# Performance work log

Hardware: AMD Instinct MI355X
Metric: run time of the kernel (lower is better)

Reference implementation:

```python
import jax, jax.numpy as jnp
import numpy as np

IN_FEATURES = 5
OUT_FEATURES = 10
BITS = 2
N_TOKENS = 4_000_000


def fake_quant_weight(w, bits):
    # Symmetric per-output-channel quantization.
    # levels: qmin = -2^(b-1), qmax = 2^(b-1)-1  (for bits=2: {-2,-1,0,1})
    qmax = 2 ** (bits - 1) - 1
    qmin = -(2 ** (bits - 1))
    # per-row (per output channel) scale; avoid div-by-zero
    scale = jnp.max(jnp.abs(w), axis=1, keepdims=True) / qmax  # [out, 1]
    scale = jnp.maximum(scale, 1e-8)
    w_q = jnp.clip(jnp.round(w / scale), qmin, qmax)
    return w_q * scale  # dequantized weight, [out, in]


def setup_inputs() -> dict:
    key = jax.random.key(0)
    kx, kw, kb = jax.random.split(key, 3)
    x = jax.random.normal(kx, (N_TOKENS, IN_FEATURES), dtype=jnp.float32)
    # Kaiming-uniform-ish init like nn.Linear
    bound = 1.0 / np.sqrt(IN_FEATURES)
    weight = jax.random.uniform(kw, (OUT_FEATURES, IN_FEATURES), dtype=jnp.float32,
                                minval=-bound, maxval=bound)
    bias = jax.random.uniform(kb, (OUT_FEATURES,), dtype=jnp.float32,
                              minval=-bound, maxval=bound)
    return {"x": x, "weight": weight, "bias": bias}


def reference(x, weight, bias):
    # QuantizedLinear(5, 10, bits=2): 2-bit fake-quantized weight matmul + bias.
    w_deq = fake_quant_weight(weight, BITS)            # [out, in]
    return x @ w_deq.T + bias                          # [N, out]
```

## Files before the change

### kernel.cpp

```cpp
#include <hip/hip_runtime.h>


constexpr int IN_F = 5;
constexpr int OUT_F = 10;
constexpr int BLOCK = 256;
constexpr int TOK_PER_TILE = 1024;

__global__ __launch_bounds__(BLOCK) void qlinear_kernel(
    const float* __restrict__ x,
    const float* __restrict__ w,
    const float* __restrict__ bias,
    float* __restrict__ out,
    int n_tokens)
{
    __shared__ float wdq[OUT_F * IN_F];
    __shared__ float bsh[OUT_F];
    __shared__ float xs[TOK_PER_TILE * IN_F];
    __shared__ float os[TOK_PER_TILE * OUT_F];

    const int tid = threadIdx.x;

    if (tid < OUT_F) {
        float row[IN_F];
        float mx = 0.0f;
        #pragma unroll
        for (int j = 0; j < IN_F; ++j) {
            row[j] = w[tid * IN_F + j];
            mx = fmaxf(mx, fabsf(row[j]));
        }
        float scale = fmaxf(mx, 1e-8f);
        #pragma unroll
        for (int j = 0; j < IN_F; ++j) {
            float q = rintf(row[j] / scale);
            q = fminf(fmaxf(q, -2.0f), 1.0f);
            wdq[tid * IN_F + j] = q * scale;
        }
        bsh[tid] = bias[tid];
    }
    __syncthreads();

    const long tok0 = (long)blockIdx.x * TOK_PER_TILE;
    const bool full = (tok0 + TOK_PER_TILE) <= (long)n_tokens;

    const long xbase = tok0 * IN_F;
    if (full) {
        const float4* __restrict__ xg = (const float4*)(x + xbase);
        float4* xls = (float4*)xs;
        #pragma unroll
        for (int k = 0; k < (TOK_PER_TILE * IN_F / 4) / BLOCK; ++k)
            xls[tid + k * BLOCK] = xg[tid + k * BLOCK];
    } else {
        const long xtotal = (long)n_tokens * IN_F;
        for (int k = tid; k < TOK_PER_TILE * IN_F; k += BLOCK) {
            long gi = xbase + k;
            xs[k] = (gi < xtotal) ? x[gi] : 0.0f;
        }
    }
    __syncthreads();

    #pragma unroll
    for (int m = 0; m < TOK_PER_TILE / BLOCK; ++m) {
        const int lt = tid + m * BLOCK;
        float xv[IN_F];
        #pragma unroll
        for (int j = 0; j < IN_F; ++j) xv[j] = xs[lt * IN_F + j];
        #pragma unroll
        for (int o = 0; o < OUT_F; ++o) {
            float acc = bsh[o];
            #pragma unroll
            for (int j = 0; j < IN_F; ++j)
                acc = fmaf(xv[j], wdq[o * IN_F + j], acc);
            os[lt * OUT_F + o] = acc;
        }
    }
    __syncthreads();

    const long obase = tok0 * OUT_F;
    if (full) {
        const float4* ols = (const float4*)os;
        float4* __restrict__ og = (float4*)(out + obase);
        #pragma unroll
        for (int k = 0; k < (TOK_PER_TILE * OUT_F / 4) / BLOCK; ++k)
            og[tid + k * BLOCK] = ols[tid + k * BLOCK];
    } else {
        const long ototal = (long)n_tokens * OUT_F;
        for (int k = tid; k < TOK_PER_TILE * OUT_F; k += BLOCK) {
            long gi = obase + k;
            if (gi < ototal) out[gi] = os[k];
        }
    }
}

extern "C" void kernel_launch(void* const* d_in, const int* in_sizes, int n_in,
                              void* d_out, int out_size, void* d_ws, size_t ws_size,
                              hipStream_t stream) {
    const float* x    = (const float*)d_in[0];
    const float* wgt  = (const float*)d_in[1];
    const float* bias = (const float*)d_in[2];
    float* out = (float*)d_out;

    const int n_tokens = in_sizes[0] / IN_F;
    const int tiles = (n_tokens + TOK_PER_TILE - 1) / TOK_PER_TILE;

    qlinear_kernel<<<tiles, BLOCK, 0, stream>>>(x, wgt, bias, out, n_tokens);
}
```

Measured before the change: 225.0 us.

## Replace shared-memory tiling with per-thread two-token register computation

Removes the shared-memory staging of input and output tiles and has each thread load two tokens' inputs directly with float2 loads, compute both outputs in registers, and write them with float4 stores. This aims to cut the large LDS footprint that limited occupancy and to eliminate block barriers. Global accesses become strided per thread rather than fully coalesced, and an odd trailing token would no longer be processed.

```diff
diff --git a/kernel.cpp b/kernel.cpp
--- a/kernel.cpp
+++ b/kernel.cpp
@@ -1,94 +1,73 @@
 #include <hip/hip_runtime.h>
 
 
-constexpr int IN_F = 5;
+constexpr int IN_F  = 5;
 constexpr int OUT_F = 10;
 constexpr int BLOCK = 256;
-constexpr int TOK_PER_TILE = 1024;
 
 __global__ __launch_bounds__(BLOCK) void qlinear_kernel(
     const float* __restrict__ x,
     const float* __restrict__ w,
     const float* __restrict__ bias,
     float* __restrict__ out,
-    int n_tokens)
+    int n_pairs)
 {
     __shared__ float wdq[OUT_F * IN_F];
     __shared__ float bsh[OUT_F];
-    __shared__ float xs[TOK_PER_TILE * IN_F];
-    __shared__ float os[TOK_PER_TILE * OUT_F];
 
-    const int tid = threadIdx.x;
-
-    if (tid < OUT_F) {
+    if (threadIdx.x < OUT_F) {
+        const int o = threadIdx.x;
         float row[IN_F];
         float mx = 0.0f;
         #pragma unroll
         for (int j = 0; j < IN_F; ++j) {
-            row[j] = w[tid * IN_F + j];
+            row[j] = w[o * IN_F + j];
             mx = fmaxf(mx, fabsf(row[j]));
         }
-        float scale = fmaxf(mx, 1e-8f);
+        const float scale = fmaxf(mx, 1e-8f);
         #pragma unroll
         for (int j = 0; j < IN_F; ++j) {
             float q = rintf(row[j] / scale);
             q = fminf(fmaxf(q, -2.0f), 1.0f);
-            wdq[tid * IN_F + j] = q * scale;
+            wdq[o * IN_F + j] = q * scale;
         }
-        bsh[tid] = bias[tid];
+        bsh[o] = bias[o];
     }
     __syncthreads();
 
-    const long tok0 = (long)blockIdx.x * TOK_PER_TILE;
-    const bool full = (tok0 + TOK_PER_TILE) <= (long)n_tokens;
+    const int p = blockIdx.x * BLOCK + threadIdx.x;
+    if (p >= n_pairs) return;
 
-    const long xbase = tok0 * IN_F;
-    if (full) {
-        const float4* __restrict__ xg = (const float4*)(x + xbase);
-        float4* xls = (float4*)xs;
+    const float2* __restrict__ xg = (const float2*)(x + (long)p * (2 * IN_F));
+    float xv[2 * IN_F];
+    #pragma unroll
+    for (int k = 0; k < IN_F; ++k) {
+        float2 v = xg[k];
+        xv[2 * k]     = v.x;
+        xv[2 * k + 1] = v.y;
+    }
+
+    float o0[OUT_F], o1[OUT_F];
+    #pragma unroll
+    for (int o = 0; o < OUT_F; ++o) {
+        float a0 = bsh[o];
+        float a1 = a0;
         #pragma unroll
-        for (int k = 0; k < (TOK_PER_TILE * IN_F / 4) / BLOCK; ++k)
-            xls[tid + k * BLOCK] = xg[tid + k * BLOCK];
-    } else {
-        const long xtotal = (long)n_tokens * IN_F;
-        for (int k = tid; k < TOK_PER_TILE * IN_F; k += BLOCK) {
-            long gi = xbase + k;
-            xs[k] = (gi < xtotal) ? x[gi] : 0.0f;
+        for (int j = 0; j < IN_F; ++j) {
+            const float wv = wdq[o * IN_F + j];
+            a0 = fmaf(xv[j],         wv, a0);
+            a1 = fmaf(xv[IN_F + j],  wv, a1);
         }
+        o0[o] = a0;
+        o1[o] = a1;
     }
-    __syncthreads();
 
-    #pragma unroll
-    for (int m = 0; m < TOK_PER_TILE / BLOCK; ++m) {
-        const int lt = tid + m * BLOCK;
-        float xv[IN_F];
-        #pragma unroll
-        for (int j = 0; j < IN_F; ++j) xv[j] = xs[lt * IN_F + j];
-        #pragma unroll
-        for (int o = 0; o < OUT_F; ++o) {
-            float acc = bsh[o];
-            #pragma unroll
-            for (int j = 0; j < IN_F; ++j)
-                acc = fmaf(xv[j], wdq[o * IN_F + j], acc);
-            os[lt * OUT_F + o] = acc;
-        }
-    }
-    __syncthreads();
-
-    const long obase = tok0 * OUT_F;
-    if (full) {
-        const float4* ols = (const float4*)os;
-        float4* __restrict__ og = (float4*)(out + obase);
-        #pragma unroll
-        for (int k = 0; k < (TOK_PER_TILE * OUT_F / 4) / BLOCK; ++k)
-            og[tid + k * BLOCK] = ols[tid + k * BLOCK];
-    } else {
-        const long ototal = (long)n_tokens * OUT_F;
-        for (int k = tid; k < TOK_PER_TILE * OUT_F; k += BLOCK) {
-            long gi = obase + k;
-            if (gi < ototal) out[gi] = os[k];
-        }
-    }
+    float4* __restrict__ og = (float4*)(out + (long)p * (2 * OUT_F));
+    og[0] = make_float4(o0[0], o0[1], o0[2], o0[3]);
+    og[1] = make_float4(o0[4], o0[5], o0[6], o0[7]);
+    og[2] = make_float4(o0[8], o0[9], o1[0], o1[1]);
+    og[3] = make_float4(o1[2], o1[3], o1[4], o1[5]);
+    og[4] = make_float4(o1[6], o1[7], o1[8], o1[9]);
 }
 
 extern "C" void kernel_launch(void* const* d_in, const int* in_sizes, int n_in,
@@ -100,7 +79,8 @@
     float* out = (float*)d_out;
 
     const int n_tokens = in_sizes[0] / IN_F;
-    const int tiles = (n_tokens + TOK_PER_TILE - 1) / TOK_PER_TILE;
+    const int n_pairs  = n_tokens / 2;
+    const int blocks   = (n_pairs + BLOCK - 1) / BLOCK;
 
-    qlinear_kernel<<<tiles, BLOCK, 0, stream>>>(x, wgt, bias, out, n_tokens);
+    qlinear_kernel<<<blocks, BLOCK, 0, stream>>>(x, wgt, bias, out, n_pairs);
 }
```

Measured after the change: 236.7 us. +5.2%, slower.

## Shrink tiles to one token per thread and use nontemporal scalar accesses

Applied to the files above, without the earlier changes.

Cuts the per-block tile from 1024 to 256 tokens, so each thread handles a single token. This reduces shared memory per block from about 60KB to about 15KB, which should let many more blocks stay resident per CU and hide memory latency better. Global loads and stores become scalar nontemporal accesses instead of float4 copies, to keep streaming data out of the cache. The separate barrier after the weight dequantization is folded into the barrier after the x load. The tradeoffs are narrower memory instructions, more blocks to launch and the weight preprocessing being repeated in four times as many blocks.

```diff
diff --git a/kernel.cpp b/kernel.cpp
--- a/kernel.cpp
+++ b/kernel.cpp
@@ -1,10 +1,10 @@
 #include <hip/hip_runtime.h>
 
 
-constexpr int IN_F = 5;
+constexpr int IN_F  = 5;
 constexpr int OUT_F = 10;
 constexpr int BLOCK = 256;
-constexpr int TOK_PER_TILE = 1024;
+constexpr int TOK   = 256;
 
 __global__ __launch_bounds__(BLOCK) void qlinear_kernel(
     const float* __restrict__ x,
@@ -15,8 +15,8 @@
 {
     __shared__ float wdq[OUT_F * IN_F];
     __shared__ float bsh[OUT_F];
-    __shared__ float xs[TOK_PER_TILE * IN_F];
-    __shared__ float os[TOK_PER_TILE * OUT_F];
+    __shared__ float xs[TOK * IN_F];
+    __shared__ float os[TOK * OUT_F];
 
     const int tid = threadIdx.x;
 
@@ -28,7 +28,7 @@
             row[j] = w[tid * IN_F + j];
             mx = fmaxf(mx, fabsf(row[j]));
         }
-        float scale = fmaxf(mx, 1e-8f);
+        const float scale = fmaxf(mx, 1e-8f);
         #pragma unroll
         for (int j = 0; j < IN_F; ++j) {
             float q = rintf(row[j] / scale);
@@ -37,55 +37,56 @@
         }
         bsh[tid] = bias[tid];
     }
-    __syncthreads();
 
-    const long tok0 = (long)blockIdx.x * TOK_PER_TILE;
-    const bool full = (tok0 + TOK_PER_TILE) <= (long)n_tokens;
+    const long tok0 = (long)blockIdx.x * TOK;
+    const bool full = (tok0 + TOK) <= (long)n_tokens;
+    const long xbase = tok0 * IN_F;
+    const long obase = tok0 * OUT_F;
 
-    const long xbase = tok0 * IN_F;
     if (full) {
-        const float4* __restrict__ xg = (const float4*)(x + xbase);
-        float4* xls = (float4*)xs;
         #pragma unroll
-        for (int k = 0; k < (TOK_PER_TILE * IN_F / 4) / BLOCK; ++k)
-            xls[tid + k * BLOCK] = xg[tid + k * BLOCK];
+        for (int i = 0; i < IN_F; ++i) {
+            const int k = i * BLOCK + tid;
+            xs[k] = __builtin_nontemporal_load(x + xbase + k);
+        }
     } else {
         const long xtotal = (long)n_tokens * IN_F;
-        for (int k = tid; k < TOK_PER_TILE * IN_F; k += BLOCK) {
-            long gi = xbase + k;
+        #pragma unroll
+        for (int i = 0; i < IN_F; ++i) {
+            const int k = i * BLOCK + tid;
+            const long gi = xbase + k;
             xs[k] = (gi < xtotal) ? x[gi] : 0.0f;
         }
     }
     __syncthreads();
 
-    #pragma unroll
-    for (int m = 0; m < TOK_PER_TILE / BLOCK; ++m) {
-        const int lt = tid + m * BLOCK;
+    {
         float xv[IN_F];
         #pragma unroll
-        for (int j = 0; j < IN_F; ++j) xv[j] = xs[lt * IN_F + j];
+        for (int j = 0; j < IN_F; ++j) xv[j] = xs[tid * IN_F + j];
         #pragma unroll
         for (int o = 0; o < OUT_F; ++o) {
             float acc = bsh[o];
             #pragma unroll
             for (int j = 0; j < IN_F; ++j)
                 acc = fmaf(xv[j], wdq[o * IN_F + j], acc);
-            os[lt * OUT_F + o] = acc;
+            os[tid * OUT_F + o] = acc;
         }
     }
     __syncthreads();
 
-    const long obase = tok0 * OUT_F;
     if (full) {
-        const float4* ols = (const float4*)os;
-        float4* __restrict__ og = (float4*)(out + obase);
         #pragma unroll
-        for (int k = 0; k < (TOK_PER_TILE * OUT_F / 4) / BLOCK; ++k)
-            og[tid + k * BLOCK] = ols[tid + k * BLOCK];
+        for (int i = 0; i < OUT_F; ++i) {
+            const int k = i * BLOCK + tid;
+            __builtin_nontemporal_store(os[k], out + obase + k);
+        }
     } else {
         const long ototal = (long)n_tokens * OUT_F;
-        for (int k = tid; k < TOK_PER_TILE * OUT_F; k += BLOCK) {
-            long gi = obase + k;
+        #pragma unroll
+        for (int i = 0; i < OUT_F; ++i) {
+            const int k = i * BLOCK + tid;
+            const long gi = obase + k;
             if (gi < ototal) out[gi] = os[k];
         }
     }
@@ -100,7 +101,7 @@
     float* out = (float*)d_out;
 
     const int n_tokens = in_sizes[0] / IN_F;
-    const int tiles = (n_tokens + TOK_PER_TILE - 1) / TOK_PER_TILE;
+    const int blocks   = (n_tokens + TOK - 1) / TOK;
 
-    qlinear_kernel<<<tiles, BLOCK, 0, stream>>>(x, wgt, bias, out, n_tokens);
+    qlinear_kernel<<<blocks, BLOCK, 0, stream>>>(x, wgt, bias, out, n_tokens);
 }
```

Result: faster. 212.4 us (-5.6%).
